# Kernel tuning notes

Measured on AMD Instinct MI355X. Metric: run time of the kernel, lower is better.

## Reference

```python
import jax, jax.numpy as jnp
import numpy as np

N_ENT = 50000
N_REL = 500
N_EDGE = 640000
D_IN = 128
D_OUT = 128
NEG_SLOPE = 0.01  # torch nn.LeakyReLU default
BN_EPS = 1e-5


def setup_inputs() -> dict:
    key = jax.random.key(0)
    ks = jax.random.split(key, 16)
    edge_index = jax.random.randint(ks[0], (2, N_EDGE), 0, N_ENT)
    edge_type = jax.random.randint(ks[1], (N_EDGE,), 0, N_REL)
    query_type = jax.random.randint(ks[2], (N_EDGE,), 0, N_REL)
    entity_embed = jax.random.normal(ks[3], (N_ENT, D_IN), jnp.float32)
    rel_embed = jax.random.normal(ks[4], (N_REL, D_IN), jnp.float32)
    s = 0.05
    return {
        "edge_index": edge_index,
        "edge_type": edge_type,
        "query_type": query_type,
        "entity_embed": entity_embed,
        "rel_embed": rel_embed,
        "w_loop": jax.random.normal(ks[5], (D_IN, D_OUT), jnp.float32) * s,
        "w_out": jax.random.normal(ks[6], (D_IN, D_OUT), jnp.float32) * s,
        "w_rel": jax.random.normal(ks[7], (D_IN, D_OUT), jnp.float32) * s,
        "loop_rel": jax.random.normal(ks[8], (1, D_IN), jnp.float32) * s,
        "W_w": jax.random.normal(ks[9], (D_IN, D_IN), jnp.float32) * s,   # W.weight^T layout: x @ W_w
        "W_b": jnp.zeros((D_IN,), jnp.float32),
        "a_w": jax.random.normal(ks[10], (2 * D_IN, 1), jnp.float32) * s,
        "a_b": jnp.zeros((1,), jnp.float32),
        "bias": jnp.zeros((D_OUT,), jnp.float32),
        "bn_gamma": jnp.ones((D_OUT,), jnp.float32),
        "bn_beta": jnp.zeros((D_OUT,), jnp.float32),
    }


def _compgcn_fwd(edge_index, edge_type, query_type, entity_embed, rel_embed,
                 w_loop, w_out, w_rel, loop_rel, W_w, W_b, a_w, a_b,
                 bias, bn_gamma, bn_beta):
    N = entity_embed.shape[0]
    rel_all = jnp.concatenate([rel_embed, loop_rel], axis=0)  # (R+1, D)
    row, col = edge_index[0], edge_index[1]  # values already in [0, N)

    # edge norm: 1/out-degree of source node (deg[row] >= 1 for every edge)
    deg = jax.ops.segment_sum(jnp.ones((row.shape[0],), entity_embed.dtype), row, num_segments=N)
    norm = 1.0 / deg[row]  # (E,)

    # self-loop branch (mode='loop'): rel_transform 'mult' with loop relation, no attention
    loop_res = (entity_embed * rel_all[-1]) @ w_loop  # (N, D_out)

    # out branch (mode='out')
    x_j = entity_embed[col]          # (E, D)
    r_e = rel_all[edge_type]         # (E, D)
    q_e = rel_all[query_type]        # (E, D)
    xj_rel = x_j * r_e               # 'mult' composition

    h = jnp.concatenate([r_e @ W_w + W_b, q_e @ W_w + W_b], axis=-1)  # (E, 2D)
    logits = h @ a_w + a_b                                            # (E, 1)
    alpha = jnp.exp(jax.nn.leaky_relu(logits[:, 0], NEG_SLOPE))       # (E,)
    sum_alpha = jax.ops.segment_sum(alpha, row, num_segments=N)       # (N,)
    alpha = alpha / sum_alpha[row]

    msg = (xj_rel @ w_out) * (alpha * norm)[:, None]                  # (E, D_out)
    out_res = jax.ops.segment_sum(msg, row, num_segments=N)           # (N, D_out)

    out = 0.5 * out_res + 0.5 * loop_res + bias  # dropout = identity (eval)
    # BatchNorm1d, training-mode batch statistics (biased var), over node dim
    mean = jnp.mean(out, axis=0)
    var = jnp.mean((out - mean) ** 2, axis=0)
    out = (out - mean) * jax.lax.rsqrt(var + BN_EPS) * bn_gamma + bn_beta

    ent_out = jax.nn.leaky_relu(out, NEG_SLOPE)
    rel_out = (rel_all @ w_rel)[:-1]
    return ent_out, rel_out


def reference(edge_index, edge_type, query_type, entity_embed, rel_embed,
              w_loop, w_out, w_rel, loop_rel, W_w, W_b, a_w, a_b,
              bias, bn_gamma, bn_beta):
    return _compgcn_fwd(edge_index, edge_type, query_type, entity_embed, rel_embed,
                        w_loop, w_out, w_rel, loop_rel, W_w, W_b, a_w, a_b,
                        bias, bn_gamma, bn_beta)
```

## Files before the change

kernel.cpp:

```cpp
#include <hip/hip_runtime.h>
#include <math.h>

#define E_N 640000
#define N_N 50000
#define R_N 500
#define D   128
#define NEG 0.01f
#define BNEPS 1e-5f
#define CAP 48

typedef __bf16 bf16x8 __attribute__((ext_vector_type(8)));
typedef float f32x4 __attribute__((ext_vector_type(4)));

#define CNT_OFF    0u
#define STAT_OFF   50000u
#define ZERO_FLOATS 50256u
#define BUCKET_OFF 50256u
#define ENTBF_OFF  4850256u
#define RELBF_OFF  8050256u
#define BT_OFF     8082256u
#define S1_OFF     8098640u
#define S2_OFF     8099152u

__device__ __forceinline__ float lrelu(float x) { return x > 0.f ? x : NEG * x; }

__device__ __forceinline__ void st_bf16x4(__bf16* p, float x, float y, float z, float w) {
    union { __bf16 b[4]; uint2 u; } pk;
    pk.b[0] = (__bf16)x; pk.b[1] = (__bf16)y; pk.b[2] = (__bf16)z; pk.b[3] = (__bf16)w;
    *(uint2*)p = pk.u;
}

__device__ __forceinline__ void st_bf16x8(__bf16* p, const float* v) {
    union { __bf16 b[8]; uint4 u; } pk;
#pragma unroll
    for (int j = 0; j < 8; ++j) pk.b[j] = (__bf16)v[j];
    *(uint4*)p = pk.u;
}

__device__ __forceinline__ void fma8(uint4 ue, uint4 ur, float a, float* acc) {
    const unsigned* we = (const unsigned*)&ue;
    const unsigned* wr = (const unsigned*)&ur;
#pragma unroll
    for (int w = 0; w < 4; ++w) {
        float e_lo = __uint_as_float(we[w] << 16);
        float e_hi = __uint_as_float(we[w] & 0xffff0000u);
        float r_lo = __uint_as_float(wr[w] << 16);
        float r_hi = __uint_as_float(wr[w] & 0xffff0000u);
        acc[2 * w]     = fmaf(a * e_lo, r_lo, acc[2 * w]);
        acc[2 * w + 1] = fmaf(a * e_hi, r_hi, acc[2 * w + 1]);
    }
}

#define PREP_S   501
#define PREP_WB  256
#define PREP_REL 500
#define PREP_ENT 3125

__global__ __launch_bounds__(128) void k_prep(const float* __restrict__ Ww,
                                              const float* __restrict__ Wb,
                                              const float* __restrict__ aw,
                                              const float* __restrict__ rel,
                                              const float* __restrict__ looprel,
                                              const float* __restrict__ wout,
                                              const float* __restrict__ wloop,
                                              const float* __restrict__ wrel,
                                              const float* __restrict__ ent,
                                              float* __restrict__ s1,
                                              float* __restrict__ s2,
                                              __bf16* __restrict__ Bt,
                                              float* __restrict__ out_rel,
                                              __bf16* __restrict__ ent_bf,
                                              __bf16* __restrict__ rel_bf) {
    int b = blockIdx.x, t = threadIdx.x;
    if (b < PREP_S) {
        __shared__ float rr[D];
        __shared__ float part[4];
        const float* rp = (b < R_N) ? rel + (size_t)b * D : looprel;
        rr[t] = rp[t];
        if (b < R_N) rel_bf[(size_t)b * D + t] = (__bf16)rp[t];
        __syncthreads();
        float v = 0.f;
        for (int i = 0; i < D; ++i) v = fmaf(rr[i], Ww[i * D + t], v);
        float p1 = aw[t] * v + Wb[t] * aw[t];
        float p2 = aw[D + t] * v + Wb[t] * aw[D + t];
        for (int o = 32; o; o >>= 1) {
            p1 += __shfl_down(p1, o);
            p2 += __shfl_down(p2, o);
        }
        if ((t & 63) == 0) {
            part[(t >> 6) * 2] = p1;
            part[(t >> 6) * 2 + 1] = p2;
        }
        __syncthreads();
        if (t == 0) {
            s1[b] = part[0] + part[2];
            s2[b] = part[1] + part[3];
        }
    } else if (b < PREP_S + PREP_WB) {
        int idx = (b - PREP_S) * 128 + t;
        int n = idx & 127, k = idx >> 7;
        float v = (k < D) ? wout[(size_t)k * D + n] : wloop[(size_t)(k - D) * D + n];
        Bt[(size_t)n * 256 + k] = (__bf16)v;
    } else if (b < PREP_S + PREP_WB + PREP_REL) {
        int r = b - (PREP_S + PREP_WB);
        __shared__ float rr2[D];
        rr2[t] = rel[(size_t)r * D + t];
        __syncthreads();
        float a = 0.f;
        for (int k = 0; k < D; ++k) a = fmaf(rr2[k], wrel[(size_t)k * D + t], a);
        out_rel[(size_t)r * D + t] = a;
    } else {
        int blk = b - (PREP_S + PREP_WB + PREP_REL);
        const float4* e4 = (const float4*)ent;
#pragma unroll
        for (int j = 0; j < 4; ++j) {
            int idx = blk * 512 + j * 128 + t;
            float4 v = e4[idx];
            st_bf16x4(ent_bf + (size_t)idx * 4, v.x, v.y, v.z, v.w);
        }
    }
}

__global__ __launch_bounds__(256) void k_bin(const int* __restrict__ row,
                                             const int* __restrict__ col,
                                             const int* __restrict__ et,
                                             const int* __restrict__ qt,
                                             int* __restrict__ cnt,
                                             int2* __restrict__ bucket) {
    int e = blockIdx.x * blockDim.x + threadIdx.x;
    if (e >= E_N) return;
    int r = row[e];
    int pos = atomicAdd(&cnt[r], 1);
    if (pos < CAP) {
        bucket[(size_t)r * CAP + pos] = make_int2(col[e], et[e] | (qt[e] << 16));
    }
}

__global__ __launch_bounds__(128) void k_gather(const int* __restrict__ cnt,
                                                const int2* __restrict__ bucket,
                                                const float* __restrict__ s1,
                                                const float* __restrict__ s2,
                                                const float* __restrict__ ab,
                                                const __bf16* __restrict__ ent_bf,
                                                const __bf16* __restrict__ rel_bf,
                                                const float* __restrict__ looprel,
                                                __bf16* __restrict__ stage) {
    int n = blockIdx.x, t = threadIdx.x;
    int deg = cnt[n];
    int m = deg < CAP ? deg : CAP;
    __shared__ int eoff[CAP];
    __shared__ int roff[CAP];
    __shared__ float sa[CAP];
    __shared__ float xred[16][8];
    if (t < m) {
        int2 be = bucket[(size_t)n * CAP + t];
        eoff[t] = be.x << 8;
        int e_t = be.y & 0xffff;
        int q_t = be.y >> 16;
        roff[t] = e_t << 8;
        sa[t] = expf(lrelu(s1[e_t] + s2[q_t] + ab[0]));
    }
    __syncthreads();
    float suma = 0.f;
    for (int i = 0; i < m; ++i) suma += sa[i];
    int s = t & 15, g = t >> 4;
    const char* eb = (const char*)ent_bf;
    const char* rb = (const char*)rel_bf;
    int co = s * 16;
    float acc[8] = {0, 0, 0, 0, 0, 0, 0, 0};
    float acc2[8] = {0, 0, 0, 0, 0, 0, 0, 0};
    for (int i = 0; i < m; i += 16) {
        int e0 = i + g, e1 = i + g + 8;
        if (e0 < m) {
            uint4 ue = *(const uint4*)(eb + (eoff[e0] + co));
            uint4 ur = *(const uint4*)(rb + (roff[e0] + co));
            fma8(ue, ur, sa[e0], acc);
        }
        if (e1 < m) {
            uint4 ue = *(const uint4*)(eb + (eoff[e1] + co));
            uint4 ur = *(const uint4*)(rb + (roff[e1] + co));
            fma8(ue, ur, sa[e1], acc2);
        }
    }
#pragma unroll
    for (int k = 0; k < 8; ++k) {
        acc[k] += acc2[k];
        acc[k] += __shfl_xor(acc[k], 16);
        acc[k] += __shfl_xor(acc[k], 32);
    }
    if (t >= 64 && t < 80) {
#pragma unroll
        for (int k = 0; k < 8; ++k) xred[s][k] = acc[k];
    }
    if (t >= 96 && t < 112) {
        int si = t - 96;
        uint4 ue = *(const uint4*)(eb + ((size_t)n << 8) + si * 16);
        const unsigned* we = (const unsigned*)&ue;
        float v[8];
#pragma unroll
        for (int w = 0; w < 4; ++w) {
            v[2 * w]     = __uint_as_float(we[w] << 16) * looprel[si * 8 + 2 * w];
            v[2 * w + 1] = __uint_as_float(we[w] & 0xffff0000u) * looprel[si * 8 + 2 * w + 1];
        }
        st_bf16x8(stage + (size_t)n * 256 + 128 + si * 8, v);
    }
    __syncthreads();
    if (t < 16) {
        float inv = (deg > 0) ? 1.0f / (suma * (float)deg) : 0.f;
        float v[8];
#pragma unroll
        for (int k = 0; k < 8; ++k) v[k] = (acc[k] + xred[s][k]) * inv;
        st_bf16x8(stage + (size_t)n * 256 + s * 8, v);
    }
}

__global__ __launch_bounds__(256) void k_gemm(const __bf16* stage,
                                              const __bf16* __restrict__ Bt,
                                              const float* __restrict__ bias,
                                              float* out,
                                              float* __restrict__ stat) {
    int t = threadIdx.x;
    int wave = t >> 6, l = t & 63;
    int lm = l & 15, lg = l >> 4;
    size_t mbase = (size_t)blockIdx.x * 128 + wave * 32;
    const bf16x8* A = (const bf16x8*)stage;
    const bf16x8* B = (const bf16x8*)Bt;
    f32x4 acc[2][8];
#pragma unroll
    for (int mt = 0; mt < 2; ++mt)
#pragma unroll
        for (int nt = 0; nt < 8; ++nt) acc[mt][nt] = (f32x4)(0.f);
#pragma unroll
    for (int ks = 0; ks < 8; ++ks) {
        bf16x8 a0 = A[(mbase + lm) * 32 + ks * 4 + lg];
        bf16x8 a1 = A[(mbase + 16 + lm) * 32 + ks * 4 + lg];
#pragma unroll
        for (int nt = 0; nt < 8; ++nt) {
            bf16x8 b = B[(size_t)(nt * 16 + lm) * 32 + ks * 4 + lg];
            acc[0][nt] = __builtin_amdgcn_mfma_f32_16x16x32_bf16(a0, b, acc[0][nt], 0, 0, 0);
            acc[1][nt] = __builtin_amdgcn_mfma_f32_16x16x32_bf16(a1, b, acc[1][nt], 0, 0, 0);
        }
    }
    float psum[8], psq[8];
#pragma unroll
    for (int nt = 0; nt < 8; ++nt) { psum[nt] = 0.f; psq[nt] = 0.f; }
#pragma unroll
    for (int mt = 0; mt < 2; ++mt) {
#pragma unroll
        for (int nt = 0; nt < 8; ++nt) {
            int c = nt * 16 + lm;
            float bv = bias[c];
#pragma unroll
            for (int r = 0; r < 4; ++r) {
                size_t rowi = mbase + mt * 16 + lg * 4 + r;
                if (rowi < N_N) {
                    float v = 0.5f * acc[mt][nt][r] + bv;
                    out[rowi * D + c] = v;
                    psum[nt] += v;
                    psq[nt] += v * v;
                }
            }
        }
    }
    __shared__ float2 red[8][16][16];
    int slot = wave * 4 + lg;
#pragma unroll
    for (int nt = 0; nt < 8; ++nt) red[nt][lm][slot] = make_float2(psum[nt], psq[nt]);
    __syncthreads();
    if (t < 128) {
        int nt = t >> 4, lmm = t & 15;
        float ss = 0.f, qq = 0.f;
#pragma unroll
        for (int k = 0; k < 16; ++k) {
            float2 v = red[nt][lmm][k];
            ss += v.x;
            qq += v.y;
        }
        atomicAdd(&stat[t], ss);
        atomicAdd(&stat[D + t], qq);
    }
}

__global__ __launch_bounds__(256) void k_bnapply(float* __restrict__ out,
                                                 const float* __restrict__ stat,
                                                 const float* __restrict__ gamma,
                                                 const float* __restrict__ beta) {
    __shared__ float ssc[D], ssh[D];
    int t = threadIdx.x;
    if (t < D) {
        float mean = stat[t] * (1.0f / N_N);
        float var = stat[D + t] * (1.0f / N_N) - mean * mean;
        float sc = gamma[t] * rsqrtf(var + BNEPS);
        ssc[t] = sc;
        ssh[t] = beta[t] - mean * sc;
    }
    __syncthreads();
    const float4* sc4 = (const float4*)ssc;
    const float4* sh4 = (const float4*)ssh;
    float4* o4 = (float4*)out;
    const int total = N_N * D / 4;
    for (int i = blockIdx.x * blockDim.x + t; i < total; i += gridDim.x * blockDim.x) {
        int d4 = i & 31;
        float4 v = o4[i];
        float4 s = sc4[d4];
        float4 h = sh4[d4];
        v.x = lrelu(v.x * s.x + h.x);
        v.y = lrelu(v.y * s.y + h.y);
        v.z = lrelu(v.z * s.z + h.z);
        v.w = lrelu(v.w * s.w + h.w);
        o4[i] = v;
    }
}

extern "C" void kernel_launch(void* const* d_in, const int* in_sizes, int n_in,
                              void* d_out, int out_size, void* d_ws, size_t ws_size,
                              hipStream_t stream) {
    const int* edge_index = (const int*)d_in[0];
    const int* row = edge_index;
    const int* col = edge_index + E_N;
    const int* etype = (const int*)d_in[1];
    const int* qtype = (const int*)d_in[2];
    const float* ent = (const float*)d_in[3];
    const float* rel = (const float*)d_in[4];
    const float* w_loop = (const float*)d_in[5];
    const float* w_out = (const float*)d_in[6];
    const float* w_rel = (const float*)d_in[7];
    const float* loop_rel = (const float*)d_in[8];
    const float* W_w = (const float*)d_in[9];
    const float* W_b = (const float*)d_in[10];
    const float* a_w = (const float*)d_in[11];
    const float* a_b = (const float*)d_in[12];
    const float* bias = (const float*)d_in[13];
    const float* bn_gamma = (const float*)d_in[14];
    const float* bn_beta = (const float*)d_in[15];

    float* ws = (float*)d_ws;
    int* cnt = (int*)(ws + CNT_OFF);
    float* stat = ws + STAT_OFF;
    int2* bucket = (int2*)(ws + BUCKET_OFF);
    __bf16* ent_bf = (__bf16*)(ws + ENTBF_OFF);
    __bf16* rel_bf = (__bf16*)(ws + RELBF_OFF);
    __bf16* Bt = (__bf16*)(ws + BT_OFF);
    float* s1 = ws + S1_OFF;
    float* s2 = ws + S2_OFF;

    float* out_ent = (float*)d_out;
    float* out_rel = out_ent + (size_t)N_N * D;
    __bf16* stage = (__bf16*)d_out;

    hipMemsetAsync(d_ws, 0, (size_t)ZERO_FLOATS * sizeof(float), stream);

    k_prep<<<PREP_S + PREP_WB + PREP_REL + PREP_ENT, 128, 0, stream>>>(
        W_w, W_b, a_w, rel, loop_rel, w_out, w_loop, w_rel, ent,
        s1, s2, Bt, out_rel, ent_bf, rel_bf);
    k_bin<<<(E_N + 255) / 256, 256, 0, stream>>>(row, col, etype, qtype, cnt, bucket);
    k_gather<<<N_N, 128, 0, stream>>>(cnt, bucket, s1, s2, a_b, ent_bf, rel_bf,
                                      loop_rel, stage);
    k_gemm<<<(N_N + 127) / 128, 256, 0, stream>>>(stage, Bt, bias, out_ent, stat);
    k_bnapply<<<2048, 256, 0, stream>>>(out_ent, stat, bn_gamma, bn_beta);
}
```

Baseline: 146.3 us.

## Compute attention weights and their sums during binning, unroll fixed-cap gather loop

Splits the prep kernel so the relation-side scores are ready first. Binning is then fused with the bf16 entity conversion, and each edge's exp attention weight is computed at binning time. The weight is stored in the bucket and summed per node with float atomics, so the gather kernel no longer does the exp or the serial per-node sum. The gather edge loop is fully unrolled to the cap of 48, with zero-padded slots. The cost is an extra atomic per edge, and column and edge type are packed into 16 bits each, which assumes indices below 65536.

```diff
diff --git a/kernel.cpp b/kernel.cpp
--- a/kernel.cpp
+++ b/kernel.cpp
@@ -13,14 +13,15 @@
 typedef float f32x4 __attribute__((ext_vector_type(4)));
 
 #define CNT_OFF    0u
-#define STAT_OFF   50000u
-#define ZERO_FLOATS 50256u
-#define BUCKET_OFF 50256u
-#define ENTBF_OFF  4850256u
-#define RELBF_OFF  8050256u
-#define BT_OFF     8082256u
-#define S1_OFF     8098640u
-#define S2_OFF     8099152u
+#define SUMA_OFF   50000u
+#define STAT_OFF   100000u
+#define ZERO_FLOATS 100256u
+#define BUCKET_OFF 100256u
+#define ENTBF_OFF  4900256u
+#define RELBF_OFF  8100256u
+#define BT_OFF     8132256u
+#define S1_OFF     8148640u
+#define S2_OFF     8149152u
 
 __device__ __forceinline__ float lrelu(float x) { return x > 0.f ? x : NEG * x; }
 
@@ -51,12 +52,11 @@
     }
 }
 
-#define PREP_S   501
-#define PREP_WB  256
-#define PREP_REL 500
-#define PREP_ENT 3125
-
-__global__ __launch_bounds__(128) void k_prep(const float* __restrict__ Ww,
+#define P1_S   501
+#define P1_WB  256
+#define P1_REL 500
+
+__global__ __launch_bounds__(128) void k_pre1(const float* __restrict__ Ww,
                                               const float* __restrict__ Wb,
                                               const float* __restrict__ aw,
                                               const float* __restrict__ rel,
@@ -64,15 +64,13 @@
                                               const float* __restrict__ wout,
                                               const float* __restrict__ wloop,
                                               const float* __restrict__ wrel,
-                                              const float* __restrict__ ent,
                                               float* __restrict__ s1,
                                               float* __restrict__ s2,
                                               __bf16* __restrict__ Bt,
                                               float* __restrict__ out_rel,
-                                              __bf16* __restrict__ ent_bf,
                                               __bf16* __restrict__ rel_bf) {
     int b = blockIdx.x, t = threadIdx.x;
-    if (b < PREP_S) {
+    if (b < P1_S) {
         __shared__ float rr[D];
         __shared__ float part[4];
         const float* rp = (b < R_N) ? rel + (size_t)b * D : looprel;
@@ -96,51 +94,65 @@
             s1[b] = part[0] + part[2];
             s2[b] = part[1] + part[3];
         }
-    } else if (b < PREP_S + PREP_WB) {
-        int idx = (b - PREP_S) * 128 + t;
+    } else if (b < P1_S + P1_WB) {
+        int idx = (b - P1_S) * 128 + t;
         int n = idx & 127, k = idx >> 7;
         float v = (k < D) ? wout[(size_t)k * D + n] : wloop[(size_t)(k - D) * D + n];
         Bt[(size_t)n * 256 + k] = (__bf16)v;
-    } else if (b < PREP_S + PREP_WB + PREP_REL) {
-        int r = b - (PREP_S + PREP_WB);
+    } else {
+        int r = b - (P1_S + P1_WB);
         __shared__ float rr2[D];
         rr2[t] = rel[(size_t)r * D + t];
         __syncthreads();
         float a = 0.f;
         for (int k = 0; k < D; ++k) a = fmaf(rr2[k], wrel[(size_t)k * D + t], a);
         out_rel[(size_t)r * D + t] = a;
+    }
+}
+
+#define P2_BIN 2500
+#define P2_ENT 1563
+
+__global__ __launch_bounds__(256) void k_pre2(const int* __restrict__ row,
+                                              const int* __restrict__ col,
+                                              const int* __restrict__ et,
+                                              const int* __restrict__ qt,
+                                              const float* __restrict__ s1,
+                                              const float* __restrict__ s2,
+                                              const float* __restrict__ ab,
+                                              const float* __restrict__ ent,
+                                              int* __restrict__ cnt,
+                                              float* __restrict__ suma,
+                                              int2* __restrict__ bucket,
+                                              __bf16* __restrict__ ent_bf) {
+    int b = blockIdx.x, t = threadIdx.x;
+    if (b < P2_BIN) {
+        int e = b * 256 + t;
+        int r = row[e];
+        float a = __expf(lrelu(s1[et[e]] + s2[qt[e]] + ab[0]));
+        atomicAdd(&suma[r], a);
+        int pos = atomicAdd(&cnt[r], 1);
+        if (pos < CAP) {
+            bucket[(size_t)r * CAP + pos] =
+                make_int2(col[e] | (et[e] << 16), __float_as_int(a));
+        }
     } else {
-        int blk = b - (PREP_S + PREP_WB + PREP_REL);
+        int blk = b - P2_BIN;
         const float4* e4 = (const float4*)ent;
 #pragma unroll
         for (int j = 0; j < 4; ++j) {
-            int idx = blk * 512 + j * 128 + t;
-            float4 v = e4[idx];
-            st_bf16x4(ent_bf + (size_t)idx * 4, v.x, v.y, v.z, v.w);
-        }
-    }
-}
-
-__global__ __launch_bounds__(256) void k_bin(const int* __restrict__ row,
-                                             const int* __restrict__ col,
-                                             const int* __restrict__ et,
-                                             const int* __restrict__ qt,
-                                             int* __restrict__ cnt,
-                                             int2* __restrict__ bucket) {
-    int e = blockIdx.x * blockDim.x + threadIdx.x;
-    if (e >= E_N) return;
-    int r = row[e];
-    int pos = atomicAdd(&cnt[r], 1);
-    if (pos < CAP) {
-        bucket[(size_t)r * CAP + pos] = make_int2(col[e], et[e] | (qt[e] << 16));
+            int idx = blk * 1024 + j * 256 + t;
+            if (idx < N_N * D / 4) {
+                float4 v = e4[idx];
+                st_bf16x4(ent_bf + (size_t)idx * 4, v.x, v.y, v.z, v.w);
+            }
+        }
     }
 }
 
 __global__ __launch_bounds__(128) void k_gather(const int* __restrict__ cnt,
+                                                const float* __restrict__ suma,
                                                 const int2* __restrict__ bucket,
-                                                const float* __restrict__ s1,
-                                                const float* __restrict__ s2,
-                                                const float* __restrict__ ab,
                                                 const __bf16* __restrict__ ent_bf,
                                                 const __bf16* __restrict__ rel_bf,
                                                 const float* __restrict__ looprel,
@@ -152,39 +164,32 @@
     __shared__ int roff[CAP];
     __shared__ float sa[CAP];
     __shared__ float xred[16][8];
-    if (t < m) {
-        int2 be = bucket[(size_t)n * CAP + t];
-        eoff[t] = be.x << 8;
-        int e_t = be.y & 0xffff;
-        int q_t = be.y >> 16;
-        roff[t] = e_t << 8;
-        sa[t] = expf(lrelu(s1[e_t] + s2[q_t] + ab[0]));
+    if (t < CAP) {
+        if (t < m) {
+            int2 be = bucket[(size_t)n * CAP + t];
+            eoff[t] = (be.x & 0xffff) << 8;
+            roff[t] = (be.x >> 16) << 8;
+            sa[t] = __int_as_float(be.y);
+        } else {
+            eoff[t] = 0; roff[t] = 0; sa[t] = 0.f;
+        }
     }
     __syncthreads();
-    float suma = 0.f;
-    for (int i = 0; i < m; ++i) suma += sa[i];
     int s = t & 15, g = t >> 4;
     const char* eb = (const char*)ent_bf;
     const char* rb = (const char*)rel_bf;
     int co = s * 16;
     float acc[8] = {0, 0, 0, 0, 0, 0, 0, 0};
-    float acc2[8] = {0, 0, 0, 0, 0, 0, 0, 0};
-    for (int i = 0; i < m; i += 16) {
-        int e0 = i + g, e1 = i + g + 8;
-        if (e0 < m) {
-            uint4 ue = *(const uint4*)(eb + (eoff[e0] + co));
-            uint4 ur = *(const uint4*)(rb + (roff[e0] + co));
-            fma8(ue, ur, sa[e0], acc);
-        }
-        if (e1 < m) {
-            uint4 ue = *(const uint4*)(eb + (eoff[e1] + co));
-            uint4 ur = *(const uint4*)(rb + (roff[e1] + co));
-            fma8(ue, ur, sa[e1], acc2);
-        }
-    }
+#define EDGE(e_) { \
+        uint4 ue = *(const uint4*)(eb + (eoff[e_] + co)); \
+        uint4 ur = *(const uint4*)(rb + (roff[e_] + co)); \
+        fma8(ue, ur, sa[e_], acc); }
+    EDGE(g) EDGE(g + 8)
+    if (m > 16) { EDGE(g + 16) EDGE(g + 24) }
+    if (m > 32) { EDGE(g + 32) EDGE(g + 40) }
+#undef EDGE
 #pragma unroll
     for (int k = 0; k < 8; ++k) {
-        acc[k] += acc2[k];
         acc[k] += __shfl_xor(acc[k], 16);
         acc[k] += __shfl_xor(acc[k], 32);
     }
@@ -206,7 +211,7 @@
     }
     __syncthreads();
     if (t < 16) {
-        float inv = (deg > 0) ? 1.0f / (suma * (float)deg) : 0.f;
+        float inv = (deg > 0) ? 1.0f / (suma[n] * (float)deg) : 0.f;
         float v[8];
 #pragma unroll
         for (int k = 0; k < 8; ++k) v[k] = (acc[k] + xred[s][k]) * inv;
@@ -336,6 +341,7 @@
 
     float* ws = (float*)d_ws;
     int* cnt = (int*)(ws + CNT_OFF);
+    float* suma = ws + SUMA_OFF;
     float* stat = ws + STAT_OFF;
     int2* bucket = (int2*)(ws + BUCKET_OFF);
     __bf16* ent_bf = (__bf16*)(ws + ENTBF_OFF);
@@ -350,12 +356,13 @@
 
     hipMemsetAsync(d_ws, 0, (size_t)ZERO_FLOATS * sizeof(float), stream);
 
-    k_prep<<<PREP_S + PREP_WB + PREP_REL + PREP_ENT, 128, 0, stream>>>(
-        W_w, W_b, a_w, rel, loop_rel, w_out, w_loop, w_rel, ent,
-        s1, s2, Bt, out_rel, ent_bf, rel_bf);
-    k_bin<<<(E_N + 255) / 256, 256, 0, stream>>>(row, col, etype, qtype, cnt, bucket);
-    k_gather<<<N_N, 128, 0, stream>>>(cnt, bucket, s1, s2, a_b, ent_bf, rel_bf,
-                                      loop_rel, stage);
+    k_pre1<<<P1_S + P1_WB + P1_REL, 128, 0, stream>>>(
+        W_w, W_b, a_w, rel, loop_rel, w_out, w_loop, w_rel,
+        s1, s2, Bt, out_rel, rel_bf);
+    k_pre2<<<P2_BIN + P2_ENT, 256, 0, stream>>>(
+        row, col, etype, qtype, s1, s2, a_b, ent, cnt, suma, bucket, ent_bf);
+    k_gather<<<N_N, 128, 0, stream>>>(cnt, suma, bucket, ent_bf, rel_bf, loop_rel,
+                                      stage);
     k_gemm<<<(N_N + 127) / 128, 256, 0, stream>>>(stage, Bt, bias, out_ent, stat);
     k_bnapply<<<2048, 256, 0, stream>>>(out_ent, stat, bn_gamma, bn_beta);
 }
```

New measurement: 172.1 us. +17.6%, slower.
